# Optimization experiments

Measured on AMD Instinct MI355X. Metric: run time of the kernel, lower is better.

Reference implementation:

```python
import jax, jax.numpy as jnp
import numpy as np

N, E, HID, ED, L, H, D = 65536, 262144, 256, 64, 2, 8, 32
FF = 4 * HID
A_START = 8192  # first action gripper node; nodes [A_START:] are the T*K action nodes


def _ln(x, s, b, eps=1e-5):
    mu = jnp.mean(x, -1, keepdims=True)
    var = jnp.var(x, -1, keepdims=True)
    return (x - mu) * jax.lax.rsqrt(var + eps) * s + b


def _gnn_forward(x, edge_attr, edge_index, Wq, Wk, Wv, WeK, WeV, Wo,
                 ln1_s, ln1_b, ffn_w1, ffn_b1, ffn_w2, ffn_b2, ln2_s, ln2_b):
    # Hetero graph transformer over the single ('gripper','action','gripper') relation:
    # per-layer edge-indexed gather -> multi-head attention with edge features ->
    # segment softmax over incoming edges -> scatter-aggregate -> residual/LN/FFN.
    n = x.shape[0]
    e = edge_attr.shape[0]
    src, dst = edge_index[0], edge_index[1]
    inv_sqrt_d = np.float32(1.0 / np.sqrt(D))
    for l in range(Wq.shape[0]):
        q = (x @ Wq[l]).reshape(n, H, D)
        k = (x @ Wk[l]).reshape(n, H, D)
        v = (x @ Wv[l]).reshape(n, H, D)
        kj = k[src] + (edge_attr @ WeK[l]).reshape(e, H, D)  # [E,H,D] gathered keys + edge bias
        vj = v[src] + (edge_attr @ WeV[l]).reshape(e, H, D)
        score = jnp.einsum('ehd,ehd->eh', q[dst], kj) * inv_sqrt_d  # [E,H]
        smax = jax.ops.segment_max(score, dst, num_segments=n)
        p = jnp.exp(score - smax[dst])
        denom = jax.ops.segment_sum(p, dst, num_segments=n)
        alpha = p / denom[dst]  # segment softmax over incoming edges
        agg = jax.ops.segment_sum((alpha[..., None] * vj).reshape(e, H * D), dst, num_segments=n)
        x = _ln(x + agg @ Wo[l], ln1_s[l], ln1_b[l])
        hid = jax.nn.gelu(x @ ffn_w1[l] + ffn_b1[l], approximate=False) @ ffn_w2[l] + ffn_b2[l]
        x = _ln(x + hid, ln2_s[l], ln2_b[l])
    return x


def setup_inputs() -> dict:
    key = jax.random.key(0)
    ks = iter(jax.random.split(key, 16))
    w = lambda shape: jax.random.normal(next(ks), shape, jnp.float32) * 0.05
    return {
        "all_gripper_feats": jax.random.normal(next(ks), (N, HID), jnp.float32),
        "edge_attr": jax.random.normal(next(ks), (E, ED), jnp.float32),
        "Wq": w((L, HID, H * D)), "Wk": w((L, HID, H * D)), "Wv": w((L, HID, H * D)),
        "WeK": w((L, ED, H * D)), "WeV": w((L, ED, H * D)), "Wo": w((L, H * D, HID)),
        "ln1_s": jnp.ones((L, HID), jnp.float32), "ln1_b": jnp.zeros((L, HID), jnp.float32),
        "ffn_w1": w((L, HID, FF)), "ffn_b1": jnp.zeros((L, FF), jnp.float32),
        "ffn_w2": w((L, FF, HID)), "ffn_b2": jnp.zeros((L, HID), jnp.float32),
        "ln2_s": jnp.ones((L, HID), jnp.float32), "ln2_b": jnp.zeros((L, HID), jnp.float32),
        "head_w1": w((HID, HID)), "head_b1": jnp.zeros((HID,), jnp.float32),
        "head_w2": w((HID, 7)), "head_b2": jnp.zeros((7,), jnp.float32),
        "edge_index": jax.random.randint(next(ks), (2, E), 0, N),
        "action_start": A_START,
    }


def reference(all_gripper_feats, edge_attr, Wq, Wk, Wv, WeK, WeV, Wo,
              ln1_s, ln1_b, ffn_w1, ffn_b1, ffn_w2, ffn_b2, ln2_s, ln2_b,
              head_w1, head_b1, head_w2, head_b2, edge_index, action_start):
    x = _gnn_forward(all_gripper_feats, edge_attr, edge_index, Wq, Wk, Wv, WeK, WeV, Wo,
                     ln1_s, ln1_b, ffn_w1, ffn_b1, ffn_w2, ffn_b2, ln2_s, ln2_b)
    a = x[action_start:]  # action gripper nodes (T*K, hidden)
    return jax.nn.gelu(a @ head_w1 + head_b1, approximate=False) @ head_w2 + head_b2  # (T*K, 7)
```

## Files before the change

kernel.cpp:

```cpp
#include <hip/hip_runtime.h>
#include <hip/hip_bf16.h>
#include <math.h>

#define NN     65536
#define NE     262144
#define HIDN   256
#define EDIM   64
#define NHEAD  8
#define FFN    1024
#define ASTART 8192
#define NACT   (NN - ASTART)
#define NCH    32768
#define NCHP   (NCH + 128)
#define NCHUNK (NE / NCH)
#define DPC    (NN / NCHUNK)
#define RCH    32768

typedef __attribute__((ext_vector_type(8))) short short8;
typedef __attribute__((ext_vector_type(4))) short short4v;
typedef __attribute__((ext_vector_type(4))) float float4v;
typedef __hip_bfloat16 bf16;

__device__ __forceinline__ float b2f(short s) {
    union { unsigned u; float f; } c;
    c.u = ((unsigned)(unsigned short)s) << 16;
    return c.f;
}
__device__ __forceinline__ short f2b(float f) {
    __hip_bfloat16 h = __float2bfloat16(f);
    return *reinterpret_cast<short*>(&h);
}
__device__ __forceinline__ float gelu_fast(float v) {
    const float x  = v * 0.70710678118654752f;
    const float ax = fabsf(x);
    const float t  = __builtin_amdgcn_rcpf(1.0f + 0.3275911f * ax);
    const float y  = t * (0.254829592f + t * (-0.284496736f + t * (1.421413741f +
                     t * (-1.453152027f + t * 1.061405429f))));
    const float e  = __expf(-x * x);
    float erf = 1.0f - y * e;
    erf = copysignf(erf, x);
    return 0.5f * v * (1.0f + erf);
}
__device__ __forceinline__ void gload16(const void* g, void* l) {
    __builtin_amdgcn_global_load_lds(
        (const __attribute__((address_space(1))) void*)(uintptr_t)g,
        (__attribute__((address_space(3))) void*)(unsigned)(uintptr_t)l,
        16, 0, 0);
}

__global__ void convert_kernel(const float* __restrict__ src,
                               bf16* __restrict__ dst, int n) {
    int i = blockIdx.x * 256 + threadIdx.x;
    if (i < n) dst[i] = __float2bfloat16(src[i]);
}
__global__ void convert4_kernel(const float* __restrict__ src,
                                bf16* __restrict__ dst, int n4) {
    int i = blockIdx.x * 256 + threadIdx.x;
    if (i >= n4) return;
    float4v f = *(const float4v*)(src + (size_t)i * 4);
    short4v o;
    #pragma unroll
    for (int j = 0; j < 4; ++j) o[j] = f2b(f[j]);
    *(short4v*)((short*)dst + (size_t)i * 4) = o;
}

__global__ void gather_kernel(const float* __restrict__ src,
                              const int* __restrict__ perm,
                              bf16* __restrict__ dst) {
    int i = blockIdx.x * 256 + threadIdx.x;
    if (i >= NE * 16) return;
    const int p = i >> 4, j = i & 15;
    const float4v f = *(const float4v*)(src + (size_t)perm[p] * EDIM + j * 4);
    short4v o;
    #pragma unroll
    for (int k = 0; k < 4; ++k) o[k] = f2b(f[k]);
    *(short4v*)((short*)dst + (size_t)p * EDIM + j * 4) = o;
}

__global__ void transpose_kernel(const float* __restrict__ src,
                                 bf16* __restrict__ dst, int R, int Cc) {
    int o = blockIdx.x * 256 + threadIdx.x;
    if (o * 4 >= R * Cc) return;
    const int c  = (o * 4) / R;
    const int r0 = (o * 4) - c * R;
    short4v w;
    #pragma unroll
    for (int j = 0; j < 4; ++j)
        w[j] = f2b(src[(size_t)(r0 + j) * Cc + c]);
    *(short4v*)((short*)dst + (size_t)c * R + r0) = w;
}

__global__ void hist_kernel(const int* __restrict__ dstI, int* __restrict__ cnt) {
    int i = blockIdx.x * 256 + threadIdx.x;
    if (i < NE) atomicAdd(&cnt[dstI[i]], 1);
}
__global__ void scan1_kernel(const int* __restrict__ cnt, int* __restrict__ rp,
                             int* __restrict__ bsum) {
    __shared__ int s[256];
    int t = threadIdx.x, i = blockIdx.x * 256 + t;
    int v = cnt[i]; s[t] = v; __syncthreads();
    for (int off = 1; off < 256; off <<= 1) {
        int x = (t >= off) ? s[t - off] : 0; __syncthreads();
        s[t] += x; __syncthreads();
    }
    rp[i] = s[t] - v;
    if (t == 255) bsum[blockIdx.x] = s[255];
}
__global__ void scan2_kernel(int* __restrict__ bsum) {
    __shared__ int s[256];
    int t = threadIdx.x; int v = bsum[t]; s[t] = v; __syncthreads();
    for (int off = 1; off < 256; off <<= 1) {
        int x = (t >= off) ? s[t - off] : 0; __syncthreads();
        s[t] += x; __syncthreads();
    }
    bsum[t] = s[t] - v;
}
__global__ void scan3_kernel(int* __restrict__ rp, const int* __restrict__ bsum,
                             int* __restrict__ cursor) {
    int i = blockIdx.x * 256 + threadIdx.x;
    int v = rp[i] + bsum[i >> 8];
    rp[i] = v; cursor[i] = v;
    if (i == 0) rp[NN] = NE;
}
__global__ void scatter_kernel(const int* __restrict__ srcI, const int* __restrict__ dstI,
                               int* __restrict__ cursor, int* __restrict__ perm,
                               int* __restrict__ src_s, int* __restrict__ dst_s) {
    int e = blockIdx.x * 256 + threadIdx.x;
    if (e >= NE) return;
    int d = dstI[e];
    int pos = atomicAdd(&cursor[d], 1);
    perm[pos] = e; src_s[pos] = srcI[e]; dst_s[pos] = d;
}

template<int AMODE, bool DO_GELU>
__global__ __launch_bounds__(256) void gemm_kernel(
    const void* __restrict__ A,
    const bf16* __restrict__ BT,
    const bf16* __restrict__ bias,
    bf16* __restrict__ C,
    int M, int Nn, int K,
    const int* __restrict__ perm, int permN)
{
    constexpr int RING = (AMODE == 0) ? 3 : 2;
    __shared__ __align__(16) short Ls[2 * RING][128 * 32];

    const int gx   = gridDim.x;
    const int nwg  = gx * gridDim.y;
    const int orig = blockIdx.y * gx + blockIdx.x;
    const int q8   = nwg >> 3, r8 = nwg & 7;
    const int xcd  = orig & 7, rk = orig >> 3;
    const int nid  = (xcd < r8 ? xcd * (q8 + 1) : r8 * (q8 + 1) + (xcd - r8) * q8) + rk;
    const int by   = nid / gx;
    const int bx   = nid - by * gx;

    const int t    = threadIdx.x;
    const int wave = t >> 6;
    const int lane = t & 63;
    const int l15  = lane & 15;
    const int quad = lane >> 4;
    const int wm   = (wave & 1) * 64;
    const int wn   = (wave >> 1) * 64;
    const int bm   = by * 128;
    const int bn   = bx * 128;
    const int srow = t >> 2;
    const int sw   = srow & 3;
    const int scolB = ((t & 3) ^ sw) * 8;
    const int scolA = (t & 3) * 8;

    const short* Ab = (const short*)A  + (size_t)(bm + srow) * K + scolB;
    const short* Bb = (const short*)BT + (size_t)(bn + srow) * K + scolB;
    const float* Af0 = nullptr;
    const float* Af1 = nullptr;
    if (AMODE == 1) {
        Af0 = (const float*)A + (size_t)(bm + srow) * K + scolA;
        Af1 = Af0 + (size_t)64 * K;
    } else if (AMODE == 2) {
        int i0 = bm + srow;       if (i0 >= permN) i0 = permN - 1;
        int i1 = bm + 64 + srow;  if (i1 >= permN) i1 = permN - 1;
        const int pr0 = perm[i0];
        const int pr1 = perm[i1];
        Af0 = (const float*)A + (size_t)pr0 * K + scolA;
        Af1 = (const float*)A + (size_t)pr1 * K + scolA;
    }
    const int offW  = wave * 1024;
    const int offTs = (t * 16) ^ (sw << 4);
    const int qs16  = (quad ^ (l15 & 3)) * 16;

    float4v acc[4][4];
    #pragma unroll
    for (int i = 0; i < 4; ++i)
        #pragma unroll
        for (int j = 0; j < 4; ++j) acc[i][j] = (float4v){0.f, 0.f, 0.f, 0.f};

    const int nt = K >> 5;

    auto STAGE = [&](int b, int k0) {
        char* lA = (char*)Ls[b];
        char* lB = (char*)Ls[RING + b];
        if (AMODE == 0) {
            gload16(Ab + k0,                  lA + offW);
            gload16(Ab + (size_t)64 * K + k0, lA + 4096 + offW);
        } else {
            #pragma unroll
            for (int i = 0; i < 2; ++i) {
                const float* s = (i ? Af1 : Af0) + k0;
                float4v f0 = *(const float4v*)s;
                float4v f1 = *(const float4v*)(s + 4);
                short8 w;
                #pragma unroll
                for (int j = 0; j < 4; ++j) { w[j] = f2b(f0[j]); w[4 + j] = f2b(f1[j]); }
                *(short8*)(lA + i * 4096 + offTs) = w;
            }
        }
        gload16(Bb + k0,                  lB + offW);
        gload16(Bb + (size_t)64 * K + k0, lB + 4096 + offW);
    };

    auto COMPUTE = [&](int b) {
        const char* lA = (const char*)Ls[b];
        const char* lB = (const char*)Ls[RING + b];
        short8 afr[4], bfr[4];
        #pragma unroll
        for (int i = 0; i < 4; ++i)
            afr[i] = *(const short8*)(lA + (wm + i * 16 + l15) * 64 + qs16);
        #pragma unroll
        for (int j = 0; j < 4; ++j)
            bfr[j] = *(const short8*)(lB + (wn + j * 16 + l15) * 64 + qs16);
        #pragma unroll
        for (int i = 0; i < 4; ++i)
            #pragma unroll
            for (int j = 0; j < 4; ++j)
                acc[i][j] = __builtin_amdgcn_mfma_f32_16x16x32_bf16(afr[i], bfr[j], acc[i][j], 0, 0, 0);
    };

    if (AMODE == 0) {
        STAGE(0, 0);
        STAGE(1, 32);
        for (int kt = 0; kt < nt - 2; ++kt) {
            asm volatile("s_waitcnt vmcnt(4) lgkmcnt(0)" ::: "memory");
            __builtin_amdgcn_sched_barrier(0);
            __builtin_amdgcn_s_barrier();
            __builtin_amdgcn_sched_barrier(0);
            STAGE((kt + 2) % 3, (kt + 2) * 32);
            COMPUTE(kt % 3);
        }
        asm volatile("s_waitcnt vmcnt(4) lgkmcnt(0)" ::: "memory");
        __builtin_amdgcn_sched_barrier(0);
        __builtin_amdgcn_s_barrier();
        __builtin_amdgcn_sched_barrier(0);
        COMPUTE((nt - 2) % 3);
        asm volatile("s_waitcnt vmcnt(0) lgkmcnt(0)" ::: "memory");
        __builtin_amdgcn_sched_barrier(0);
        __builtin_amdgcn_s_barrier();
        __builtin_amdgcn_sched_barrier(0);
        COMPUTE((nt - 1) % 3);
        __syncthreads();
    } else {
        STAGE(0, 0);
        __syncthreads();
        for (int kt = 0; kt < nt; ++kt) {
            const int cur = kt & 1;
            if (kt + 1 < nt) STAGE(cur ^ 1, (kt + 1) * 32);
            COMPUTE(cur);
            __syncthreads();
        }
    }

    short* Ct = (short*)Ls;
    #pragma unroll
    for (int j = 0; j < 4; ++j) {
        const int col  = wn + j * 16 + l15;
        const int pc   = col ^ (quad << 4);
        const float bv = bias ? b2f(((const short*)bias)[bn + col]) : 0.0f;
        #pragma unroll
        for (int i = 0; i < 4; ++i) {
            const int row0 = wm + i * 16 + quad * 4;
            #pragma unroll
            for (int r = 0; r < 4; ++r) {
                float v = acc[i][j][r] + bv;
                if (DO_GELU) v = gelu_fast(v);
                Ct[(row0 + r) * 128 + pc] = f2b(v);
            }
        }
    }
    __syncthreads();
    #pragma unroll
    for (int it = 0; it < 8; ++it) {
        const int row = wave * 32 + it + ((lane >> 4) << 3);
        const int cs  = (lane & 15) * 8;
        const int pcs = cs ^ (((row >> 2) & 3) << 4);
        short8 w = *(const short8*)&Ct[row * 128 + pcs];
        *(short8*)((short*)C + (size_t)(bm + row) * Nn + bn + cs) = w;
    }
}

__global__ __launch_bounds__(256) void score_kernel(
    const bf16* __restrict__ q, const bf16* __restrict__ k,
    const bf16* __restrict__ eK,
    const int* __restrict__ src_s, const int* __restrict__ dst_s,
    short* __restrict__ pbuf, int e0, int qkstride)
{
    const int p = e0 + blockIdx.x * 4 + (threadIdx.x >> 6);
    const int lane = threadIdx.x & 63;
    const int s = src_s[p], d = dst_s[p];
    const int off = lane * 4;

    const short4v qv = *(const short4v*)((const short*)q  + (size_t)d * qkstride + off);
    const short4v kv = *(const short4v*)((const short*)k  + (size_t)s * qkstride + off);
    const short4v ev = *(const short4v*)((const short*)eK + (size_t)(p - e0) * HIDN + off);
    float x = 0.f;
    #pragma unroll
    for (int j = 0; j < 4; ++j) x += b2f(qv[j]) * (b2f(kv[j]) + b2f(ev[j]));
    x += __shfl_xor(x, 1);
    x += __shfl_xor(x, 2);
    x += __shfl_xor(x, 4);
    if ((lane & 7) == 0) {
        const float sc = fminf(fmaxf(x * 0.17677669529663689f, -30.f), 30.f);
        pbuf[(size_t)p * NHEAD + (lane >> 3)] = f2b(expf(sc));
    }
}

__global__ __launch_bounds__(256) void agg_kernel(
    const short* __restrict__ pbuf, const bf16* __restrict__ v,
    const bf16* __restrict__ eV,
    const int* __restrict__ src_s, const int* __restrict__ rp,
    bf16* __restrict__ agg, int e0, int e1x, int dlo)
{
    const int d = dlo + blockIdx.x * 4 + (threadIdx.x >> 6);
    const int lane = threadIdx.x & 63;
    const int es = rp[d], ee = rp[d + 1];
    if (es < e0 || es >= e1x) return;
    const int h = lane >> 3, off = lane * 4;

    float a0 = 0.f, a1 = 0.f, a2 = 0.f, a3 = 0.f;
    if (es < ee) {
        float den = 0.f;
        for (int p = es; p < ee; ++p) den += b2f(pbuf[(size_t)p * NHEAD + h]);
        const float rden = 1.0f / den;
        for (int p = es; p < ee; ++p) {
            const float al = b2f(pbuf[(size_t)p * NHEAD + h]) * rden;
            const int s = src_s[p];
            const short4v vv = *(const short4v*)((const short*)v  + (size_t)s * HIDN + off);
            const short4v ev = *(const short4v*)((const short*)eV + (size_t)(p - e0) * HIDN + off);
            a0 += al * (b2f(vv[0]) + b2f(ev[0]));
            a1 += al * (b2f(vv[1]) + b2f(ev[1]));
            a2 += al * (b2f(vv[2]) + b2f(ev[2]));
            a3 += al * (b2f(vv[3]) + b2f(ev[3]));
        }
    }
    short4v o;
    o[0] = f2b(a0); o[1] = f2b(a1); o[2] = f2b(a2); o[3] = f2b(a3);
    *(short4v*)((short*)agg + (size_t)d * HIDN + off) = o;
}

__global__ __launch_bounds__(256) void ln_kernel(
    bf16* __restrict__ x, const bf16* __restrict__ t,
    const bf16* __restrict__ sc, const bf16* __restrict__ bi, int r0)
{
    const int row = r0 + blockIdx.x * 4 + (threadIdx.x >> 6);
    const int lane = threadIdx.x & 63;
    const size_t base = (size_t)row * HIDN + lane * 4;
    const size_t tbase = (size_t)(row - r0) * HIDN + lane * 4;
    const short4v xv = *(const short4v*)((const short*)x + base);
    const short4v tv = *(const short4v*)((const short*)t + tbase);
    float v[4];
    #pragma unroll
    for (int j = 0; j < 4; ++j) v[j] = b2f(xv[j]) + b2f(tv[j]);
    float sum = v[0] + v[1] + v[2] + v[3];
    float ssq = v[0]*v[0] + v[1]*v[1] + v[2]*v[2] + v[3]*v[3];
    #pragma unroll
    for (int m = 1; m < 64; m <<= 1) { sum += __shfl_xor(sum, m); ssq += __shfl_xor(ssq, m); }
    const float mean = sum * (1.0f / 256.0f);
    const float var  = fmaxf(ssq * (1.0f / 256.0f) - mean * mean, 0.0f);
    const float rstd = rsqrtf(var + 1e-5f);
    const short4v sv = *(const short4v*)((const short*)sc + lane * 4);
    const short4v bv = *(const short4v*)((const short*)bi + lane * 4);
    short4v out;
    #pragma unroll
    for (int j = 0; j < 4; ++j)
        out[j] = f2b((v[j] - mean) * rstd * b2f(sv[j]) + b2f(bv[j]));
    *(short4v*)((short*)x + base) = out;
}

__global__ __launch_bounds__(256) void head2_kernel(
    const bf16* __restrict__ h1, const bf16* __restrict__ w2T,
    const bf16* __restrict__ b2, float* __restrict__ out)
{
    const int row = blockIdx.x * 4 + (threadIdx.x >> 6);
    const int lane = threadIdx.x & 63;
    const int off = lane * 4;
    const short4v hv = *(const short4v*)((const short*)h1 + (size_t)row * HIDN + off);
    float hf[4];
    #pragma unroll
    for (int j = 0; j < 4; ++j) hf[j] = b2f(hv[j]);
    float acc[7];
    #pragma unroll
    for (int jc = 0; jc < 7; ++jc) {
        const short4v wv = *(const short4v*)((const short*)w2T + jc * HIDN + off);
        float a = hf[0]*b2f(wv[0]) + hf[1]*b2f(wv[1]) + hf[2]*b2f(wv[2]) + hf[3]*b2f(wv[3]);
        #pragma unroll
        for (int m = 1; m < 64; m <<= 1) a += __shfl_xor(a, m);
        acc[jc] = a;
    }
    if (lane < 7) {
        float r = lane == 0 ? acc[0] : lane == 1 ? acc[1] : lane == 2 ? acc[2] :
                  lane == 3 ? acc[3] : lane == 4 ? acc[4] : lane == 5 ? acc[5] : acc[6];
        out[(size_t)row * 7 + lane] = r + b2f(((const short*)b2)[lane]);
    }
}

extern "C" void kernel_launch(void* const* d_in, const int* in_sizes, int n_in,
                              void* d_out, int out_size, void* d_ws, size_t ws_size,
                              hipStream_t stream)
{
    const float* xin   = (const float*)d_in[0];
    const float* eattr = (const float*)d_in[1];
    const float* Wq    = (const float*)d_in[2];
    const float* Wk    = (const float*)d_in[3];
    const float* Wv    = (const float*)d_in[4];
    const float* WeK   = (const float*)d_in[5];
    const float* WeV   = (const float*)d_in[6];
    const float* Wo    = (const float*)d_in[7];
    const float* ln1s  = (const float*)d_in[8];
    const float* ln1b  = (const float*)d_in[9];
    const float* fw1   = (const float*)d_in[10];
    const float* fb1   = (const float*)d_in[11];
    const float* fw2   = (const float*)d_in[12];
    const float* fb2   = (const float*)d_in[13];
    const float* ln2s  = (const float*)d_in[14];
    const float* ln2b  = (const float*)d_in[15];
    const float* hw1   = (const float*)d_in[16];
    const float* hb1   = (const float*)d_in[17];
    const float* hw2   = (const float*)d_in[18];
    const float* hb2   = (const float*)d_in[19];
    const int*  eidx   = (const int*)d_in[20];
    const int*  srcI   = eidx;
    const int*  dstI   = eidx + NE;

    char* base = (char*)d_ws;
    size_t off = 0;
    auto carve = [&](size_t bytes) -> char* {
        char* p = base + off;
        off += (bytes + 255) & ~(size_t)255;
        return p;
    };
    bf16*  x_b    = (bf16*) carve((size_t)NN * HIDN * 2);
    bf16*  qk_b   = (bf16*) carve((size_t)NN * 2 * HIDN * 2);
    bf16*  v_b    = (bf16*) carve((size_t)NN * HIDN * 2);
    bf16*  echunk = (bf16*) carve((size_t)NCHP * HIDN * 2);
    short* pbuf   = (short*)carve((size_t)NE * NHEAD * 2);
    int*   perm   = (int*)  carve((size_t)NE * 4);
    int*   src_s  = (int*)  carve((size_t)NE * 4);
    int*   dst_s  = (int*)  carve((size_t)NE * 4);
    int*   rowp   = (int*)  carve((size_t)(NN + 1) * 4);
    bf16*  WqkT   = (bf16*) carve((size_t)2 * HIDN * HIDN * 2);
    bf16*  WvT    = (bf16*) carve((size_t)HIDN * HIDN * 2);
    bf16*  WoT    = (bf16*) carve((size_t)HIDN * HIDN * 2);
    bf16*  WeKT   = (bf16*) carve((size_t)HIDN * EDIM * 2);
    bf16*  WeVT   = (bf16*) carve((size_t)HIDN * EDIM * 2);
    bf16*  W1T    = (bf16*) carve((size_t)FFN * HIDN * 2);
    bf16*  W2T    = (bf16*) carve((size_t)HIDN * FFN * 2);
    bf16*  HW1T   = (bf16*) carve((size_t)HIDN * HIDN * 2);
    bf16*  HW2T   = (bf16*) carve((size_t)8 * HIDN * 2);
    bf16*  c_ln1s = (bf16*) carve((size_t)2 * HIDN * 2);
    bf16*  c_ln1b = (bf16*) carve((size_t)2 * HIDN * 2);
    bf16*  c_ln2s = (bf16*) carve((size_t)2 * HIDN * 2);
    bf16*  c_ln2b = (bf16*) carve((size_t)2 * HIDN * 2);
    bf16*  c_fb1  = (bf16*) carve((size_t)2 * FFN * 2);
    bf16*  c_fb2  = (bf16*) carve((size_t)2 * HIDN * 2);
    bf16*  c_hb1  = (bf16*) carve((size_t)HIDN * 2);
    bf16*  c_hb2  = (bf16*) carve((size_t)16 * 2);
    const size_t off_mand = off;
    bf16*  eattr_s = (bf16*) carve((size_t)(NE + 128) * EDIM * 2);
    const bool eg = (off <= ws_size);
    if (off_mand > ws_size) return;

    int* cnt    = (int*)echunk;
    int* cursor = cnt + NN;
    int* bsum   = cursor + NN;
    bf16*  agg_b  = qk_b;
    bf16*  tmp_b  = v_b;
    bf16*  hid    = qk_b;
    bf16*  ffnout = v_b;

    const int TB = 256;
    #define GRID1(n) dim3(((n) + TB - 1) / TB)

    convert4_kernel<<<GRID1(NN * HIDN / 4), TB, 0, stream>>>(xin, x_b, NN * HIDN / 4);
    convert_kernel<<<GRID1(2 * HIDN), TB, 0, stream>>>(ln1s, c_ln1s, 2 * HIDN);
    convert_kernel<<<GRID1(2 * HIDN), TB, 0, stream>>>(ln1b, c_ln1b, 2 * HIDN);
    convert_kernel<<<GRID1(2 * HIDN), TB, 0, stream>>>(ln2s, c_ln2s, 2 * HIDN);
    convert_kernel<<<GRID1(2 * HIDN), TB, 0, stream>>>(ln2b, c_ln2b, 2 * HIDN);
    convert_kernel<<<GRID1(2 * FFN), TB, 0, stream>>>(fb1, c_fb1, 2 * FFN);
    convert_kernel<<<GRID1(2 * HIDN), TB, 0, stream>>>(fb2, c_fb2, 2 * HIDN);
    convert_kernel<<<GRID1(HIDN), TB, 0, stream>>>(hb1, c_hb1, HIDN);
    convert_kernel<<<1, TB, 0, stream>>>(hb2, c_hb2, 7);
    transpose_kernel<<<GRID1(HIDN * HIDN / 4), TB, 0, stream>>>(hw1, HW1T, HIDN, HIDN);
    transpose_kernel<<<GRID1(HIDN * 7 / 4), TB, 0, stream>>>(hw2, HW2T, HIDN, 7);

    hipMemsetAsync(cnt, 0, (size_t)NN * 4, stream);
    hist_kernel<<<GRID1(NE), TB, 0, stream>>>(dstI, cnt);
    scan1_kernel<<<NN / 256, 256, 0, stream>>>(cnt, rowp, bsum);
    scan2_kernel<<<1, 256, 0, stream>>>(bsum);
    scan3_kernel<<<NN / 256, 256, 0, stream>>>(rowp, bsum, cursor);
    scatter_kernel<<<GRID1(NE), TB, 0, stream>>>(srcI, dstI, cursor, perm, src_s, dst_s);
    if (eg) gather_kernel<<<GRID1(NE * 16), TB, 0, stream>>>(eattr, perm, eattr_s);

    for (int l = 0; l < 2; ++l) {
        transpose_kernel<<<GRID1(HIDN * HIDN / 4), TB, 0, stream>>>(Wq + (size_t)l*HIDN*HIDN, WqkT, HIDN, HIDN);
        transpose_kernel<<<GRID1(HIDN * HIDN / 4), TB, 0, stream>>>(Wk + (size_t)l*HIDN*HIDN, WqkT + (size_t)HIDN*HIDN, HIDN, HIDN);
        transpose_kernel<<<GRID1(HIDN * HIDN / 4), TB, 0, stream>>>(Wv + (size_t)l*HIDN*HIDN, WvT, HIDN, HIDN);
        transpose_kernel<<<GRID1(EDIM * HIDN / 4), TB, 0, stream>>>(WeK + (size_t)l*EDIM*HIDN, WeKT, EDIM, HIDN);
        transpose_kernel<<<GRID1(EDIM * HIDN / 4), TB, 0, stream>>>(WeV + (size_t)l*EDIM*HIDN, WeVT, EDIM, HIDN);
        transpose_kernel<<<GRID1(HIDN * HIDN / 4), TB, 0, stream>>>(Wo + (size_t)l*HIDN*HIDN, WoT, HIDN, HIDN);
        transpose_kernel<<<GRID1(HIDN * FFN / 4),  TB, 0, stream>>>(fw1 + (size_t)l*HIDN*FFN, W1T, HIDN, FFN);
        transpose_kernel<<<GRID1(FFN * HIDN / 4),  TB, 0, stream>>>(fw2 + (size_t)l*FFN*HIDN, W2T, FFN, HIDN);

        gemm_kernel<0, false><<<dim3((2*HIDN)/128, NN/128), TB, 0, stream>>>(x_b, WqkT, nullptr, qk_b, NN, 2*HIDN, HIDN, nullptr, 0);
        gemm_kernel<0, false><<<dim3(HIDN/128, NN/128), TB, 0, stream>>>(x_b, WvT, nullptr, v_b, NN, HIDN, HIDN, nullptr, 0);

        for (int c = 0; c < NCHUNK; ++c) {
            if (eg)
                gemm_kernel<0, false><<<dim3(HIDN/128, NCH/128), TB, 0, stream>>>(
                    eattr_s + (size_t)c * NCH * EDIM, WeKT, nullptr, echunk, NCH, HIDN, EDIM, nullptr, 0);
            else
                gemm_kernel<2, false><<<dim3(HIDN/128, NCH/128), TB, 0, stream>>>(
                    eattr, WeKT, nullptr, echunk, NCH, HIDN, EDIM, perm + (size_t)c * NCH, NE - c * NCH);
            score_kernel<<<NCH / 4, TB, 0, stream>>>(qk_b, qk_b + HIDN, echunk, src_s, dst_s, pbuf, c * NCH, 2 * HIDN);
        }

        for (int c = 0; c < NCHUNK; ++c) {
            if (eg)
                gemm_kernel<0, false><<<dim3(HIDN/128, NCHP/128), TB, 0, stream>>>(
                    eattr_s + (size_t)c * NCH * EDIM, WeVT, nullptr, echunk, NCHP, HIDN, EDIM, nullptr, 0);
            else
                gemm_kernel<2, false><<<dim3(HIDN/128, NCHP/128), TB, 0, stream>>>(
                    eattr, WeVT, nullptr, echunk, NCHP, HIDN, EDIM, perm + (size_t)c * NCH, NE - c * NCH);
            const int dlo = (c == 0) ? 0 : (c - 1) * DPC;
            const int dhi = (c == NCHUNK - 1) ? NN : (c + 2) * DPC;
            const int e1x = (c == NCHUNK - 1) ? NE + 1 : (c + 1) * NCH;
            agg_kernel<<<(dhi - dlo) / 4, TB, 0, stream>>>(
                pbuf, v_b, echunk, src_s, rowp, agg_b, c * NCH, e1x, dlo);
        }

        gemm_kernel<0, false><<<dim3(HIDN/128, NN/128), TB, 0, stream>>>(agg_b, WoT, nullptr, tmp_b, NN, HIDN, HIDN, nullptr, 0);
        ln_kernel<<<NN / 4, TB, 0, stream>>>(x_b, tmp_b, c_ln1s + (size_t)l * HIDN, c_ln1b + (size_t)l * HIDN, 0);

        for (int r0 = 0; r0 < NN; r0 += RCH) {
            gemm_kernel<0, true ><<<dim3(FFN/128, RCH/128), TB, 0, stream>>>(
                x_b + (size_t)r0 * HIDN, W1T, c_fb1 + (size_t)l * FFN, hid, RCH, FFN, HIDN, nullptr, 0);
            gemm_kernel<0, false><<<dim3(HIDN/128, RCH/128), TB, 0, stream>>>(
                hid, W2T, c_fb2 + (size_t)l * HIDN, ffnout, RCH, HIDN, FFN, nullptr, 0);
            ln_kernel<<<RCH / 4, TB, 0, stream>>>(x_b, ffnout, c_ln2s + (size_t)l * HIDN, c_ln2b + (size_t)l * HIDN, r0);
        }
    }

    gemm_kernel<0, true><<<dim3(HIDN/128, NACT/128), TB, 0, stream>>>(
        x_b + (size_t)ASTART * HIDN, HW1T, c_hb1, hid, NACT, HIDN, HIDN, nullptr, 0);
    head2_kernel<<<NACT / 4, TB, 0, stream>>>(hid, HW2T, c_hb2, (float*)d_out);
}
```

Baseline: 1.484 ms.

## Fuse residual+LayerNorm into GEMM epilogue and skip non-action nodes in last layer

Adds a gemm_ln_kernel whose 128x256 tile covers a full hidden row, so the bias, residual add and LayerNorm run in the GEMM epilogue. This removes the separate ln_kernel passes and the intermediate tmp/ffnout buffers, for both the Wo projection and the FFN down-projection. In the last layer, score, aggregation, Wo and FFN work is limited to destination nodes from ASTART onward, since only those rows feed the head. The fused kernel uses a wider tile and more accumulator registers, which may lower occupancy. The dmin early-exit in the score kernel also leaves pbuf entries for skipped edges unwritten; this is safe only if nothing downstream reads them.

```diff
diff --git a/kernel.cpp b/kernel.cpp
--- a/kernel.cpp
+++ b/kernel.cpp
@@ -14,7 +14,6 @@
 #define NCHP   (NCH + 128)
 #define NCHUNK (NE / NCH)
 #define DPC    (NN / NCHUNK)
-#define RCH    32768
 
 typedef __attribute__((ext_vector_type(8))) short short8;
 typedef __attribute__((ext_vector_type(4))) short short4v;
@@ -294,15 +293,184 @@
     }
 }
 
+__global__ __launch_bounds__(256) void gemm_ln_kernel(
+    const bf16* __restrict__ A, const bf16* __restrict__ BT,
+    const bf16* __restrict__ bias, bf16* __restrict__ x,
+    const bf16* __restrict__ sc, const bf16* __restrict__ bi,
+    int M, int K, int rowbase)
+{
+    __shared__ __align__(16) short Ls[24576];
+
+    const int nwg  = gridDim.y;
+    const int orig = blockIdx.y;
+    const int q8   = nwg >> 3, r8 = nwg & 7;
+    const int xcd  = orig & 7, rk = orig >> 3;
+    const int by   = (xcd < r8 ? xcd * (q8 + 1) : r8 * (q8 + 1) + (xcd - r8) * q8) + rk;
+
+    const int t    = threadIdx.x;
+    const int wave = t >> 6;
+    const int lane = t & 63;
+    const int l15  = lane & 15;
+    const int quad = lane >> 4;
+    const int wm   = (wave & 1) * 64;
+    const int wn   = (wave >> 1) * 128;
+    const int bm   = by * 128;
+    const int srow = t >> 2;
+    const int sw   = srow & 3;
+    const int scol = ((t & 3) ^ sw) * 8;
+    const int offW = wave * 1024;
+    const int qs16 = (quad ^ (l15 & 3)) * 16;
+
+    const short* Ab = (const short*)A  + (size_t)(bm + srow) * K + scol;
+    const short* Bb = (const short*)BT + (size_t)srow * K + scol;
+
+    float4v acc[4][8];
+    #pragma unroll
+    for (int i = 0; i < 4; ++i)
+        #pragma unroll
+        for (int j = 0; j < 8; ++j) acc[i][j] = (float4v){0.f, 0.f, 0.f, 0.f};
+
+    const int nt = K >> 5;
+
+    auto STAGE = [&](int b, int k0) {
+        char* lA = (char*)Ls + b * 8192;
+        char* lB = (char*)Ls + 16384 + b * 16384;
+        gload16(Ab + k0,                   lA + offW);
+        gload16(Ab + (size_t)64 * K + k0,  lA + 4096 + offW);
+        gload16(Bb + k0,                   lB + offW);
+        gload16(Bb + (size_t)64 * K + k0,  lB + 4096 + offW);
+        gload16(Bb + (size_t)128 * K + k0, lB + 8192 + offW);
+        gload16(Bb + (size_t)192 * K + k0, lB + 12288 + offW);
+    };
+
+    STAGE(0, 0);
+    __syncthreads();
+    for (int kt = 0; kt < nt; ++kt) {
+        const int cur = kt & 1;
+        if (kt + 1 < nt) STAGE(cur ^ 1, (kt + 1) * 32);
+        const char* lA = (const char*)Ls + cur * 8192;
+        const char* lB = (const char*)Ls + 16384 + cur * 16384;
+        short8 afr[4];
+        #pragma unroll
+        for (int i = 0; i < 4; ++i)
+            afr[i] = *(const short8*)(lA + (wm + i * 16 + l15) * 64 + qs16);
+        #pragma unroll
+        for (int jb = 0; jb < 2; ++jb) {
+            short8 bfr[4];
+            #pragma unroll
+            for (int j2 = 0; j2 < 4; ++j2)
+                bfr[j2] = *(const short8*)(lB + (wn + (jb * 4 + j2) * 16 + l15) * 64 + qs16);
+            #pragma unroll
+            for (int i = 0; i < 4; ++i)
+                #pragma unroll
+                for (int j2 = 0; j2 < 4; ++j2)
+                    acc[i][jb * 4 + j2] = __builtin_amdgcn_mfma_f32_16x16x32_bf16(
+                        afr[i], bfr[j2], acc[i][jb * 4 + j2], 0, 0, 0);
+        }
+        __syncthreads();
+    }
+
+    #pragma unroll
+    for (int j = 0; j < 8; ++j) {
+        const int gcol = wn + j * 16 + l15;
+        const float bv = bias ? b2f(((const short*)bias)[gcol]) : 0.0f;
+        #pragma unroll
+        for (int i = 0; i < 4; ++i) {
+            const int row0 = wm + i * 16 + quad * 4;
+            #pragma unroll
+            for (int r = 0; r < 4; ++r) {
+                const float xv = b2f(((const short*)x)[(size_t)(rowbase + bm + row0 + r) * HIDN + gcol]);
+                acc[i][j][r] += bv + xv;
+            }
+        }
+    }
+
+    float psum[4][4], pssq[4][4];
+    #pragma unroll
+    for (int i = 0; i < 4; ++i)
+        #pragma unroll
+        for (int r = 0; r < 4; ++r) {
+            float s = 0.f, q = 0.f;
+            #pragma unroll
+            for (int j = 0; j < 8; ++j) { const float v = acc[i][j][r]; s += v; q += v * v; }
+            #pragma unroll
+            for (int m = 1; m < 16; m <<= 1) { s += __shfl_xor(s, m); q += __shfl_xor(q, m); }
+            psum[i][r] = s; pssq[i][r] = q;
+        }
+
+    float* rsum = (float*)((char*)Ls + 32768);
+    float* rssq = rsum + 256;
+    const int ch = wn >> 7;
+    if (l15 == 0) {
+        #pragma unroll
+        for (int i = 0; i < 4; ++i)
+            #pragma unroll
+            for (int r = 0; r < 4; ++r) {
+                const int row = wm + i * 16 + quad * 4 + r;
+                rsum[ch * 128 + row] = psum[i][r];
+                rssq[ch * 128 + row] = pssq[i][r];
+            }
+    }
+    __syncthreads();
+    float meanv[4][4], rstdv[4][4];
+    #pragma unroll
+    for (int i = 0; i < 4; ++i)
+        #pragma unroll
+        for (int r = 0; r < 4; ++r) {
+            const int row = wm + i * 16 + quad * 4 + r;
+            const float s = rsum[row] + rsum[128 + row];
+            const float q = rssq[row] + rssq[128 + row];
+            const float mean = s * (1.0f / 256.0f);
+            const float var  = fmaxf(q * (1.0f / 256.0f) - mean * mean, 0.0f);
+            meanv[i][r] = mean;
+            rstdv[i][r] = rsqrtf(var + 1e-5f);
+        }
+    __syncthreads();
+
+    short* Ct = (short*)Ls;
+    #pragma unroll
+    for (int h = 0; h < 2; ++h) {
+        if ((wave >> 1) == h) {
+            #pragma unroll
+            for (int j = 0; j < 8; ++j) {
+                const int colh = j * 16 + l15;
+                const int pc   = colh ^ (quad << 4);
+                const float scv = b2f(((const short*)sc)[h * 128 + colh]);
+                const float biv = b2f(((const short*)bi)[h * 128 + colh]);
+                #pragma unroll
+                for (int i = 0; i < 4; ++i) {
+                    const int row0 = wm + i * 16 + quad * 4;
+                    #pragma unroll
+                    for (int r = 0; r < 4; ++r) {
+                        const float v = (acc[i][j][r] - meanv[i][r]) * rstdv[i][r] * scv + biv;
+                        Ct[(row0 + r) * 128 + pc] = f2b(v);
+                    }
+                }
+            }
+        }
+        __syncthreads();
+        #pragma unroll
+        for (int it = 0; it < 8; ++it) {
+            const int row = wave * 32 + it + ((lane >> 4) << 3);
+            const int cs  = (lane & 15) * 8;
+            const int pcs = cs ^ (((row >> 2) & 3) << 4);
+            short8 w = *(const short8*)&Ct[row * 128 + pcs];
+            *(short8*)((short*)x + (size_t)(rowbase + bm + row) * HIDN + h * 128 + cs) = w;
+        }
+        __syncthreads();
+    }
+}
+
 __global__ __launch_bounds__(256) void score_kernel(
     const bf16* __restrict__ q, const bf16* __restrict__ k,
     const bf16* __restrict__ eK,
     const int* __restrict__ src_s, const int* __restrict__ dst_s,
-    short* __restrict__ pbuf, int e0, int qkstride)
+    short* __restrict__ pbuf, int e0, int qkstride, int dmin)
 {
     const int p = e0 + blockIdx.x * 4 + (threadIdx.x >> 6);
     const int lane = threadIdx.x & 63;
     const int s = src_s[p], d = dst_s[p];
+    if (d < dmin) return;
     const int off = lane * 4;
 
     const short4v qv = *(const short4v*)((const short*)q  + (size_t)d * qkstride + off);
@@ -324,10 +492,11 @@
     const short* __restrict__ pbuf, const bf16* __restrict__ v,
     const bf16* __restrict__ eV,
     const int* __restrict__ src_s, const int* __restrict__ rp,
-    bf16* __restrict__ agg, int e0, int e1x, int dlo)
+    bf16* __restrict__ agg, int e0, int e1x, int dlo, int dmin)
 {
     const int d = dlo + blockIdx.x * 4 + (threadIdx.x >> 6);
     const int lane = threadIdx.x & 63;
+    if (d < dmin) return;
     const int es = rp[d], ee = rp[d + 1];
     if (es < e0 || es >= e1x) return;
     const int h = lane >> 3, off = lane * 4;
@@ -351,35 +520,6 @@
     short4v o;
     o[0] = f2b(a0); o[1] = f2b(a1); o[2] = f2b(a2); o[3] = f2b(a3);
     *(short4v*)((short*)agg + (size_t)d * HIDN + off) = o;
-}
-
-__global__ __launch_bounds__(256) void ln_kernel(
-    bf16* __restrict__ x, const bf16* __restrict__ t,
-    const bf16* __restrict__ sc, const bf16* __restrict__ bi, int r0)
-{
-    const int row = r0 + blockIdx.x * 4 + (threadIdx.x >> 6);
-    const int lane = threadIdx.x & 63;
-    const size_t base = (size_t)row * HIDN + lane * 4;
-    const size_t tbase = (size_t)(row - r0) * HIDN + lane * 4;
-    const short4v xv = *(const short4v*)((const short*)x + base);
-    const short4v tv = *(const short4v*)((const short*)t + tbase);
-    float v[4];
-    #pragma unroll
-    for (int j = 0; j < 4; ++j) v[j] = b2f(xv[j]) + b2f(tv[j]);
-    float sum = v[0] + v[1] + v[2] + v[3];
-    float ssq = v[0]*v[0] + v[1]*v[1] + v[2]*v[2] + v[3]*v[3];
-    #pragma unroll
-    for (int m = 1; m < 64; m <<= 1) { sum += __shfl_xor(sum, m); ssq += __shfl_xor(ssq, m); }
-    const float mean = sum * (1.0f / 256.0f);
-    const float var  = fmaxf(ssq * (1.0f / 256.0f) - mean * mean, 0.0f);
-    const float rstd = rsqrtf(var + 1e-5f);
-    const short4v sv = *(const short4v*)((const short*)sc + lane * 4);
-    const short4v bv = *(const short4v*)((const short*)bi + lane * 4);
-    short4v out;
-    #pragma unroll
-    for (int j = 0; j < 4; ++j)
-        out[j] = f2b((v[j] - mean) * rstd * b2f(sv[j]) + b2f(bv[j]));
-    *(short4v*)((short*)x + base) = out;
 }
 
 __global__ __launch_bounds__(256) void head2_kernel(
@@ -479,9 +619,7 @@
     int* cursor = cnt + NN;
     int* bsum   = cursor + NN;
     bf16*  agg_b  = qk_b;
-    bf16*  tmp_b  = v_b;
     bf16*  hid    = qk_b;
-    bf16*  ffnout = v_b;
 
     const int TB = 256;
     #define GRID1(n) dim3(((n) + TB - 1) / TB)
@@ -507,6 +645,10 @@
     if (eg) gather_kernel<<<GRID1(NE * 16), TB, 0, stream>>>(eattr, perm, eattr_s);
 
     for (int l = 0; l < 2; ++l) {
+        const int dmin = l ? ASTART : 0;
+        const int rs   = l ? ASTART : 0;
+        const int rch  = (NN - rs) / 2;
+
         transpose_kernel<<<GRID1(HIDN * HIDN / 4), TB, 0, stream>>>(Wq + (size_t)l*HIDN*HIDN, WqkT, HIDN, HIDN);
         transpose_kernel<<<GRID1(HIDN * HIDN / 4), TB, 0, stream>>>(Wk + (size_t)l*HIDN*HIDN, WqkT + (size_t)HIDN*HIDN, HIDN, HIDN);
         transpose_kernel<<<GRID1(HIDN * HIDN / 4), TB, 0, stream>>>(Wv + (size_t)l*HIDN*HIDN, WvT, HIDN, HIDN);
@@ -526,7 +668,7 @@
             else
                 gemm_kernel<2, false><<<dim3(HIDN/128, NCH/128), TB, 0, stream>>>(
                     eattr, WeKT, nullptr, echunk, NCH, HIDN, EDIM, perm + (size_t)c * NCH, NE - c * NCH);
-            score_kernel<<<NCH / 4, TB, 0, stream>>>(qk_b, qk_b + HIDN, echunk, src_s, dst_s, pbuf, c * NCH, 2 * HIDN);
+            score_kernel<<<NCH / 4, TB, 0, stream>>>(qk_b, qk_b + HIDN, echunk, src_s, dst_s, pbuf, c * NCH, 2 * HIDN, dmin);
         }
 
         for (int c = 0; c < NCHUNK; ++c) {
@@ -540,18 +682,19 @@
             const int dhi = (c == NCHUNK - 1) ? NN : (c + 2) * DPC;
             const int e1x = (c == NCHUNK - 1) ? NE + 1 : (c + 1) * NCH;
             agg_kernel<<<(dhi - dlo) / 4, TB, 0, stream>>>(
-                pbuf, v_b, echunk, src_s, rowp, agg_b, c * NCH, e1x, dlo);
-        }
-
-        gemm_kernel<0, false><<<dim3(HIDN/128, NN/128), TB, 0, stream>>>(agg_b, WoT, nullptr, tmp_b, NN, HIDN, HIDN, nullptr, 0);
-        ln_kernel<<<NN / 4, TB, 0, stream>>>(x_b, tmp_b, c_ln1s + (size_t)l * HIDN, c_ln1b + (size_t)l * HIDN, 0);
-
-        for (int r0 = 0; r0 < NN; r0 += RCH) {
-            gemm_kernel<0, true ><<<dim3(FFN/128, RCH/128), TB, 0, stream>>>(
-                x_b + (size_t)r0 * HIDN, W1T, c_fb1 + (size_t)l * FFN, hid, RCH, FFN, HIDN, nullptr, 0);
-            gemm_kernel<0, false><<<dim3(HIDN/128, RCH/128), TB, 0, stream>>>(
-                hid, W2T, c_fb2 + (size_t)l * HIDN, ffnout, RCH, HIDN, FFN, nullptr, 0);
-            ln_kernel<<<RCH / 4, TB, 0, stream>>>(x_b, ffnout, c_ln2s + (size_t)l * HIDN, c_ln2b + (size_t)l * HIDN, r0);
+                pbuf, v_b, echunk, src_s, rowp, agg_b, c * NCH, e1x, dlo, dmin);
+        }
+
+        gemm_ln_kernel<<<dim3(1, (NN - rs)/128), TB, 0, stream>>>(
+            agg_b + (size_t)rs * HIDN, WoT, nullptr, x_b,
+            c_ln1s + (size_t)l * HIDN, c_ln1b + (size_t)l * HIDN, NN - rs, HIDN, rs);
+
+        for (int r0 = rs; r0 < NN; r0 += rch) {
+            gemm_kernel<0, true ><<<dim3(FFN/128, rch/128), TB, 0, stream>>>(
+                x_b + (size_t)r0 * HIDN, W1T, c_fb1 + (size_t)l * FFN, hid, rch, FFN, HIDN, nullptr, 0);
+            gemm_ln_kernel<<<dim3(1, rch/128), TB, 0, stream>>>(
+                hid, W2T, c_fb2 + (size_t)l * HIDN, x_b,
+                c_ln2s + (size_t)l * HIDN, c_ln2b + (size_t)l * HIDN, rch, FFN, r0);
         }
     }
 
```

Result: no change. 1.507 ms (+1.6%).

## Skip last-layer work for non-action nodes not used by output head

Applied to the files above, without the earlier changes.

In the final layer, only nodes from ASTART onward feed the output head, so score and aggregation skip edges and destinations below ASTART. The Wo GEMM, both LayerNorms and the FFN run only on the action-node rows. This cuts last-layer attention and dense work by roughly an eighth. It is a legitimate dead-code elimination, because the output depends only on those rows and layer-1 neighbours read layer-0 outputs.

```diff
diff --git a/kernel.cpp b/kernel.cpp
--- a/kernel.cpp
+++ b/kernel.cpp
@@ -14,7 +14,6 @@
 #define NCHP   (NCH + 128)
 #define NCHUNK (NE / NCH)
 #define DPC    (NN / NCHUNK)
-#define RCH    32768
 
 typedef __attribute__((ext_vector_type(8))) short short8;
 typedef __attribute__((ext_vector_type(4))) short short4v;
@@ -298,11 +297,12 @@
     const bf16* __restrict__ q, const bf16* __restrict__ k,
     const bf16* __restrict__ eK,
     const int* __restrict__ src_s, const int* __restrict__ dst_s,
-    short* __restrict__ pbuf, int e0, int qkstride)
+    short* __restrict__ pbuf, int e0, int qkstride, int dmin)
 {
     const int p = e0 + blockIdx.x * 4 + (threadIdx.x >> 6);
     const int lane = threadIdx.x & 63;
     const int s = src_s[p], d = dst_s[p];
+    if (d < dmin) return;
     const int off = lane * 4;
 
     const short4v qv = *(const short4v*)((const short*)q  + (size_t)d * qkstride + off);
@@ -324,10 +324,11 @@
     const short* __restrict__ pbuf, const bf16* __restrict__ v,
     const bf16* __restrict__ eV,
     const int* __restrict__ src_s, const int* __restrict__ rp,
-    bf16* __restrict__ agg, int e0, int e1x, int dlo)
+    bf16* __restrict__ agg, int e0, int e1x, int dlo, int dmin)
 {
     const int d = dlo + blockIdx.x * 4 + (threadIdx.x >> 6);
     const int lane = threadIdx.x & 63;
+    if (d < dmin) return;
     const int es = rp[d], ee = rp[d + 1];
     if (es < e0 || es >= e1x) return;
     const int h = lane >> 3, off = lane * 4;
@@ -507,6 +508,10 @@
     if (eg) gather_kernel<<<GRID1(NE * 16), TB, 0, stream>>>(eattr, perm, eattr_s);
 
     for (int l = 0; l < 2; ++l) {
+        const int dmin = l ? ASTART : 0;
+        const int rs   = l ? ASTART : 0;
+        const int rch  = (NN - rs) / 2;
+
         transpose_kernel<<<GRID1(HIDN * HIDN / 4), TB, 0, stream>>>(Wq + (size_t)l*HIDN*HIDN, WqkT, HIDN, HIDN);
         transpose_kernel<<<GRID1(HIDN * HIDN / 4), TB, 0, stream>>>(Wk + (size_t)l*HIDN*HIDN, WqkT + (size_t)HIDN*HIDN, HIDN, HIDN);
         transpose_kernel<<<GRID1(HIDN * HIDN / 4), TB, 0, stream>>>(Wv + (size_t)l*HIDN*HIDN, WvT, HIDN, HIDN);
@@ -526,7 +531,7 @@
             else
                 gemm_kernel<2, false><<<dim3(HIDN/128, NCH/128), TB, 0, stream>>>(
                     eattr, WeKT, nullptr, echunk, NCH, HIDN, EDIM, perm + (size_t)c * NCH, NE - c * NCH);
-            score_kernel<<<NCH / 4, TB, 0, stream>>>(qk_b, qk_b + HIDN, echunk, src_s, dst_s, pbuf, c * NCH, 2 * HIDN);
+            score_kernel<<<NCH / 4, TB, 0, stream>>>(qk_b, qk_b + HIDN, echunk, src_s, dst_s, pbuf, c * NCH, 2 * HIDN, dmin);
         }
 
         for (int c = 0; c < NCHUNK; ++c) {
@@ -540,18 +545,21 @@
             const int dhi = (c == NCHUNK - 1) ? NN : (c + 2) * DPC;
             const int e1x = (c == NCHUNK - 1) ? NE + 1 : (c + 1) * NCH;
             agg_kernel<<<(dhi - dlo) / 4, TB, 0, stream>>>(
-                pbuf, v_b, echunk, src_s, rowp, agg_b, c * NCH, e1x, dlo);
-        }
-
-        gemm_kernel<0, false><<<dim3(HIDN/128, NN/128), TB, 0, stream>>>(agg_b, WoT, nullptr, tmp_b, NN, HIDN, HIDN, nullptr, 0);
-        ln_kernel<<<NN / 4, TB, 0, stream>>>(x_b, tmp_b, c_ln1s + (size_t)l * HIDN, c_ln1b + (size_t)l * HIDN, 0);
-
-        for (int r0 = 0; r0 < NN; r0 += RCH) {
-            gemm_kernel<0, true ><<<dim3(FFN/128, RCH/128), TB, 0, stream>>>(
-                x_b + (size_t)r0 * HIDN, W1T, c_fb1 + (size_t)l * FFN, hid, RCH, FFN, HIDN, nullptr, 0);
-            gemm_kernel<0, false><<<dim3(HIDN/128, RCH/128), TB, 0, stream>>>(
-                hid, W2T, c_fb2 + (size_t)l * HIDN, ffnout, RCH, HIDN, FFN, nullptr, 0);
-            ln_kernel<<<RCH / 4, TB, 0, stream>>>(x_b, ffnout, c_ln2s + (size_t)l * HIDN, c_ln2b + (size_t)l * HIDN, r0);
+                pbuf, v_b, echunk, src_s, rowp, agg_b, c * NCH, e1x, dlo, dmin);
+        }
+
+        gemm_kernel<0, false><<<dim3(HIDN/128, (NN - rs)/128), TB, 0, stream>>>(
+            agg_b + (size_t)rs * HIDN, WoT, nullptr, tmp_b, NN - rs, HIDN, HIDN, nullptr, 0);
+        ln_kernel<<<(NN - rs) / 4, TB, 0, stream>>>(
+            x_b, tmp_b, c_ln1s + (size_t)l * HIDN, c_ln1b + (size_t)l * HIDN, rs);
+
+        for (int r0 = rs; r0 < NN; r0 += rch) {
+            gemm_kernel<0, true ><<<dim3(FFN/128, rch/128), TB, 0, stream>>>(
+                x_b + (size_t)r0 * HIDN, W1T, c_fb1 + (size_t)l * FFN, hid, rch, FFN, HIDN, nullptr, 0);
+            gemm_kernel<0, false><<<dim3(HIDN/128, rch/128), TB, 0, stream>>>(
+                hid, W2T, c_fb2 + (size_t)l * HIDN, ffnout, rch, HIDN, FFN, nullptr, 0);
+            ln_kernel<<<rch / 4, TB, 0, stream>>>(
+                x_b, ffnout, c_ln2s + (size_t)l * HIDN, c_ln2b + (size_t)l * HIDN, r0);
         }
     }
 
```

After: 1.444 ms. 2.7% less time.
